# Kernel optimization log

Hardware: AMD Instinct MI355X
Metric: run time of the kernel (lower is better)

Reference implementation:

```python
import jax, jax.numpy as jnp
import numpy as np

NUM_HEADS = 16
ROPE_BASE = 10000.0


def _rope_cos_sin(seq_len, head_dim, dtype):
    inv_freq = 1.0 / (ROPE_BASE ** (jnp.arange(0, head_dim, 2, dtype=jnp.float32) / head_dim))
    freqs = jnp.arange(seq_len, dtype=jnp.float32)[:, None] * inv_freq[None, :]  # [L, hd/2]
    return jnp.cos(freqs).astype(dtype), jnp.sin(freqs).astype(dtype)


def _apply_rope(t, cos, sin):
    # t: [B, H, L, hd]; cos/sin: [L, hd/2] broadcast over B,H
    x1 = t[..., ::2]
    x2 = t[..., 1::2]
    r1 = x1 * cos - x2 * sin
    r2 = x1 * sin + x2 * cos
    return jnp.stack([r1, r2], axis=-1).reshape(t.shape)


def setup_inputs() -> dict:
    key = jax.random.key(0)
    k1, k2, k3 = jax.random.split(key, 3)
    B, L, D = 2, 2048, 1024
    x = jax.random.normal(k1, (B, L, D), dtype=jnp.float32)
    W_qkv = jax.random.normal(k2, (3 * D, D), dtype=jnp.float32) * (D ** -0.5)
    W_out = jax.random.normal(k3, (D, D), dtype=jnp.float32) * (D ** -0.5)
    return {"x": x, "W_qkv": W_qkv, "W_out": W_out}


def reference(x, W_qkv, W_out):
    B, L, D = x.shape
    H = NUM_HEADS
    hd = D // H
    scale = hd ** -0.5

    qkv = x @ W_qkv.T                              # [B, L, 3D]
    qkv = qkv.reshape(B, L, 3, H, hd)
    qkv = jnp.transpose(qkv, (2, 0, 3, 1, 4))      # [3, B, H, L, hd]
    q, k, v = qkv[0], qkv[1], qkv[2]

    cos, sin = _rope_cos_sin(L, hd, x.dtype)
    q = _apply_rope(q, cos, sin)
    k = _apply_rope(k, cos, sin)

    logits = jnp.einsum("bhqd,bhkd->bhqk", q, k) * scale
    attn = jax.nn.softmax(logits, axis=-1)         # dropout p=0.0 -> identity
    out = jnp.einsum("bhqk,bhkd->bhqd", attn, v)   # [B, H, L, hd]
    out = jnp.transpose(out, (0, 2, 1, 3)).reshape(B, L, D)
    return out @ W_out.T
```

## Files before the change

### kernel.cpp

```cpp
#include <hip/hip_runtime.h>
#include <hip/hip_bf16.h>
#include <stdint.h>


typedef __bf16 bf16x8 __attribute__((ext_vector_type(8)));
typedef float f32x4 __attribute__((ext_vector_type(4)));

__device__ __forceinline__ unsigned short f2bf(float f) {
  union { float f; unsigned int u; } v; v.f = f;
  unsigned int r = v.u + 0x7FFFu + ((v.u >> 16) & 1u);
  return (unsigned short)(r >> 16);
}
__device__ __forceinline__ float b2f(unsigned short u) {
  union { unsigned int u; float f; } v; v.u = ((unsigned int)u) << 16;
  return v.f;
}

__device__ __forceinline__ void gl2lds16(const void* gptr, void* lptr) {
  __builtin_amdgcn_global_load_lds(
      (const __attribute__((address_space(1))) unsigned int*)gptr,
      (__attribute__((address_space(3))) unsigned int*)lptr, 16, 0, 0);
}

__global__ void cvt_all(const float4* __restrict__ x,
                        const float4* __restrict__ wq,
                        const float4* __restrict__ wo,
                        ushort4* __restrict__ xb,
                        ushort4* __restrict__ wqb,
                        ushort4* __restrict__ wob) {
  int i = blockIdx.x * 256 + threadIdx.x;
  float4 v; ushort4* dst; int j;
  if (i < 1048576)      { v = x[i];            dst = xb;  j = i; }
  else if (i < 1835008) { v = wq[i - 1048576]; dst = wqb; j = i - 1048576; }
  else                  { v = wo[i - 1835008]; dst = wob; j = i - 1835008; }
  ushort4 o;
  o.x = f2bf(v.x); o.y = f2bf(v.y); o.z = f2bf(v.z); o.w = f2bf(v.w);
  dst[j] = o;
}

template<int OUT_BF16>
__global__ __launch_bounds__(256) void gemm_bt(
    const __hip_bfloat16* __restrict__ A,
    const __hip_bfloat16* __restrict__ B,
    void* __restrict__ C, int M, int N, int K) {
  __shared__ __align__(16) __hip_bfloat16 As[128 * 32];
  __shared__ __align__(16) __hip_bfloat16 Bs[128 * 32];
  const int tid = threadIdx.x;
  const int lane = tid & 63;
  const int wave = tid >> 6;
  const int wm = (wave >> 1) * 64, wn = (wave & 1) * 64;
  const int g = lane >> 4, lr = lane & 15;
  const int m0 = blockIdx.y * 128, n0 = blockIdx.x * 128;
  f32x4 acc[4][4] = {};

  const char* Ag = (const char*)(A + (size_t)m0 * K);
  const char* Bg = (const char*)(B + (size_t)n0 * K);
  const size_t ldb = (size_t)K * 2;

  for (int kt = 0; kt < K; kt += 32) {
    const char* Ak = Ag + (size_t)kt * 2;
    const char* Bk = Bg + (size_t)kt * 2;
#pragma unroll
    for (int j = 0; j < 2; ++j) {
      int c = tid + j * 256;
      int row = c >> 2;
      int colb = (c & 3) * 16;
      gl2lds16(Ak + (size_t)row * ldb + colb, (char*)As + c * 16);
      gl2lds16(Bk + (size_t)row * ldb + colb, (char*)Bs + c * 16);
    }
    asm volatile("s_waitcnt vmcnt(0)" ::: "memory");
    __syncthreads();
    bf16x8 af[4], bfr[4];
#pragma unroll
    for (int i = 0; i < 4; ++i)
      af[i] = *(const bf16x8*)((const char*)As + (size_t)(wm + i * 16 + lr) * 64 + g * 16);
#pragma unroll
    for (int i = 0; i < 4; ++i)
      bfr[i] = *(const bf16x8*)((const char*)Bs + (size_t)(wn + i * 16 + lr) * 64 + g * 16);
#pragma unroll
    for (int i = 0; i < 4; ++i)
#pragma unroll
      for (int j = 0; j < 4; ++j)
        acc[i][j] = __builtin_amdgcn_mfma_f32_16x16x32_bf16(af[i], bfr[j], acc[i][j], 0, 0, 0);
    __syncthreads();
  }

#pragma unroll
  for (int i = 0; i < 4; ++i) {
#pragma unroll
    for (int j = 0; j < 4; ++j) {
      int n = n0 + wn + j * 16 + lr;
#pragma unroll
      for (int r = 0; r < 4; ++r) {
        int m = m0 + wm + i * 16 + g * 4 + r;
        float v = acc[i][j][r];
        if (OUT_BF16) {
          ((unsigned short*)C)[(size_t)m * N + n] = f2bf(v);
        } else {
          ((float*)C)[(size_t)m * N + n] = v;
        }
      }
    }
  }
}

__global__ void rope_scatter(const __hip_bfloat16* __restrict__ qkv,
                             __hip_bfloat16* __restrict__ Qs,
                             __hip_bfloat16* __restrict__ Ks,
                             __hip_bfloat16* __restrict__ Vt) {
  const int t = blockIdx.x * 256 + threadIdx.x;
  const int i = t & 31;
  const int lc = (t >> 5) & 255;
  const int h = (t >> 13) & 15;
  const int b = t >> 17;
  const float inv_freq = powf(10000.0f, -(float)i * (1.0f / 32.0f));
  const float QSCALE = 0.125f * 1.44269504088896f;
  const unsigned short* qk = (const unsigned short*)qkv;
  unsigned short v0[8], v1[8];
#pragma unroll
  for (int j = 0; j < 8; ++j) {
    const int l = lc * 8 + j;
    const size_t row = ((size_t)(b * 2048 + l)) * 3072;
    float s, c;
    sincosf((float)l * inv_freq, &s, &c);
    ushort2 qp = *(const ushort2*)(qk + row + h * 64 + 2 * i);
    ushort2 kp = *(const ushort2*)(qk + row + 1024 + h * 64 + 2 * i);
    ushort2 vp = *(const ushort2*)(qk + row + 2048 + h * 64 + 2 * i);
    float x1 = b2f(qp.x), x2 = b2f(qp.y);
    float y1 = b2f(kp.x), y2 = b2f(kp.y);
    size_t oidx = (((size_t)(b * 16 + h)) * 2048 + l) * 64 + 2 * i;
    ushort2 qo, ko;
    qo.x = f2bf((x1 * c - x2 * s) * QSCALE);
    qo.y = f2bf((x1 * s + x2 * c) * QSCALE);
    ko.x = f2bf(y1 * c - y2 * s);
    ko.y = f2bf(y1 * s + y2 * c);
    *(ushort2*)((unsigned short*)Qs + oidx) = qo;
    *(ushort2*)((unsigned short*)Ks + oidx) = ko;
    v0[j] = vp.x; v1[j] = vp.y;
  }
  const int m = lc & 3;
  const int colA = ((m & 1) << 4) + ((m >> 1) << 2);
  unsigned short* Vtu = (unsigned short*)Vt;
  const size_t vrow0 = (((size_t)(b * 16 + h)) * 64 + 2 * i) * 2048 + (lc >> 2) * 32;
  const size_t vrow1 = vrow0 + 2048;
  *(ushort4*)(Vtu + vrow0 + colA)     = make_ushort4(v0[0], v0[1], v0[2], v0[3]);
  *(ushort4*)(Vtu + vrow0 + colA + 8) = make_ushort4(v0[4], v0[5], v0[6], v0[7]);
  *(ushort4*)(Vtu + vrow1 + colA)     = make_ushort4(v1[0], v1[1], v1[2], v1[3]);
  *(ushort4*)(Vtu + vrow1 + colA + 8) = make_ushort4(v1[4], v1[5], v1[6], v1[7]);
}

__global__ __launch_bounds__(256, 4) void attn_fwd(
    const __hip_bfloat16* __restrict__ Qs,
    const __hip_bfloat16* __restrict__ Ks,
    const __hip_bfloat16* __restrict__ Vt,
    float* __restrict__ Opart,
    float2* __restrict__ Ml) {
  constexpr int L = 2048;
  __shared__ __align__(16) char lds[32768];
  const int tid = threadIdx.x, lane = tid & 63, w = tid >> 6;
  const int g = lane >> 4, lr = lane & 15;
  const int blk = blockIdx.x;
  const int xcd = blk & 7, slot = blk >> 3;
  const int bh = xcd * 4 + (slot >> 5);
  const int rem = slot & 31;
  const int qt = rem >> 1, half = rem & 1;
  const int q0 = qt * 128 + w * 32 + lr;
  const int kt0 = half * 16;

  const __hip_bfloat16* Qr = Qs + ((size_t)bh * L + q0) * 64;
  bf16x8 qf[2][2];
  qf[0][0] = *(const bf16x8*)(Qr + g * 8);
  qf[0][1] = *(const bf16x8*)(Qr + 32 + g * 8);
  qf[1][0] = *(const bf16x8*)(Qr + 16 * 64 + g * 8);
  qf[1][1] = *(const bf16x8*)(Qr + 16 * 64 + 32 + g * 8);

  const int xmask = (lr & 7) << 4;
  const int loff0 = ((g * 16) ^ (xmask & 0x30)) + (xmask & 0x40);
  const int kb0 = lr * 128 + loff0;
  const int kb1 = kb0 ^ 64;

  const int c0 = tid * 16, c1 = c0 + 4096;
  const int os0 = c0 ^ (((c0 >> 7) & 7) << 4);
  const int os1 = c1 ^ (((c1 >> 7) & 7) << 4);
  const char* Kb = (const char*)(Ks + (size_t)bh * L * 64) + (size_t)kt0 * 8192;
  const char* Vb = (const char*)(Vt + (size_t)bh * 64 * L) + kt0 * 128;
  const char* KsrcA = Kb + os0;
  const char* KsrcB = Kb + os1;
  const char* VsrcA = Vb + (size_t)(os0 >> 7) * (L * 2) + (os0 & 127);
  const char* VsrcB = Vb + (size_t)(os1 >> 7) * (L * 2) + (os1 & 127);

  auto stage = [&](int bo) {
    gl2lds16(KsrcA, lds + bo + c0);
    gl2lds16(KsrcB, lds + bo + c1);
    gl2lds16(VsrcA, lds + 16384 + bo + c0);
    gl2lds16(VsrcB, lds + 16384 + bo + c1);
    KsrcA += 8192; KsrcB += 8192; VsrcA += 128; VsrcB += 128;
  };

  f32x4 oacc[2][4] = {};
  float mrun[2] = {-1e30f, -1e30f}, lpart[2] = {0.0f, 0.0f};

  stage(0);

  for (int kt = 0; kt < 16; ++kt) {
    const int bo = (kt & 1) * 8192;
    if (kt + 1 < 16) {
      stage(bo ^ 8192);
      asm volatile("s_waitcnt vmcnt(4)" ::: "memory");
    } else {
      asm volatile("s_waitcnt vmcnt(0)" ::: "memory");
    }
    __builtin_amdgcn_s_barrier();

    const char* Kc = lds + bo;
    const char* Vc = lds + 16384 + bo;

    f32x4 sacc[2][4] = {};
    __builtin_amdgcn_s_setprio(1);
#pragma unroll
    for (int mf = 0; mf < 4; ++mf) {
      bf16x8 a0 = *(const bf16x8*)(Kc + kb0 + mf * 2048);
      bf16x8 a1 = *(const bf16x8*)(Kc + kb1 + mf * 2048);
      sacc[0][mf] = __builtin_amdgcn_mfma_f32_16x16x32_bf16(a0, qf[0][0], sacc[0][mf], 0, 0, 0);
      sacc[0][mf] = __builtin_amdgcn_mfma_f32_16x16x32_bf16(a1, qf[0][1], sacc[0][mf], 0, 0, 0);
      sacc[1][mf] = __builtin_amdgcn_mfma_f32_16x16x32_bf16(a0, qf[1][0], sacc[1][mf], 0, 0, 0);
      sacc[1][mf] = __builtin_amdgcn_mfma_f32_16x16x32_bf16(a1, qf[1][1], sacc[1][mf], 0, 0, 0);
    }
    __builtin_amdgcn_s_setprio(0);

#pragma unroll
    for (int qg = 0; qg < 2; ++qg) {
      float t0 = fmaxf(fmaxf(sacc[qg][0][0], sacc[qg][0][1]), fmaxf(sacc[qg][0][2], sacc[qg][0][3]));
      float t1 = fmaxf(fmaxf(sacc[qg][1][0], sacc[qg][1][1]), fmaxf(sacc[qg][1][2], sacc[qg][1][3]));
      float t2 = fmaxf(fmaxf(sacc[qg][2][0], sacc[qg][2][1]), fmaxf(sacc[qg][2][2], sacc[qg][2][3]));
      float t3 = fmaxf(fmaxf(sacc[qg][3][0], sacc[qg][3][1]), fmaxf(sacc[qg][3][2], sacc[qg][3][3]));
      float tmax = fmaxf(fmaxf(t0, t1), fmaxf(t2, t3));
      tmax = fmaxf(tmax, __shfl_xor(tmax, 16));
      tmax = fmaxf(tmax, __shfl_xor(tmax, 32));
      if (__any(tmax > mrun[qg] + 8.0f)) {
        float mnew = fmaxf(mrun[qg], tmax);
        float al = __builtin_amdgcn_exp2f(mrun[qg] - mnew);
        mrun[qg] = mnew;
        lpart[qg] *= al;
#pragma unroll
        for (int d = 0; d < 4; ++d) oacc[qg][d] = oacc[qg][d] * al;
      }
#pragma unroll
      for (int mf = 0; mf < 4; ++mf) {
        float p0 = __builtin_amdgcn_exp2f(sacc[qg][mf][0] - mrun[qg]);
        float p1 = __builtin_amdgcn_exp2f(sacc[qg][mf][1] - mrun[qg]);
        float p2 = __builtin_amdgcn_exp2f(sacc[qg][mf][2] - mrun[qg]);
        float p3 = __builtin_amdgcn_exp2f(sacc[qg][mf][3] - mrun[qg]);
        lpart[qg] += (p0 + p1) + (p2 + p3);
        sacc[qg][mf][0] = p0; sacc[qg][mf][1] = p1;
        sacc[qg][mf][2] = p2; sacc[qg][mf][3] = p3;
      }
    }

#pragma unroll
    for (int ks = 0; ks < 2; ++ks) {
      bf16x8 pf[2];
#pragma unroll
      for (int qg = 0; qg < 2; ++qg) {
#pragma unroll
        for (int j = 0; j < 4; ++j) {
          pf[qg][j]     = (__bf16)sacc[qg][2 * ks][j];
          pf[qg][4 + j] = (__bf16)sacc[qg][2 * ks + 1][j];
        }
      }
      const int kb = ks ? kb1 : kb0;
      __builtin_amdgcn_s_setprio(1);
#pragma unroll
      for (int df = 0; df < 4; ++df) {
        bf16x8 a = *(const bf16x8*)(Vc + kb + df * 2048);
        oacc[0][df] = __builtin_amdgcn_mfma_f32_16x16x32_bf16(a, pf[0], oacc[0][df], 0, 0, 0);
        oacc[1][df] = __builtin_amdgcn_mfma_f32_16x16x32_bf16(a, pf[1], oacc[1][df], 0, 0, 0);
      }
      __builtin_amdgcn_s_setprio(0);
    }
    asm volatile("s_waitcnt lgkmcnt(0)" ::: "memory");
    __builtin_amdgcn_s_barrier();
  }

#pragma unroll
  for (int qg = 0; qg < 2; ++qg) {
    float lsum = lpart[qg];
    lsum += __shfl_xor(lsum, 16);
    lsum += __shfl_xor(lsum, 32);
    const size_t rowi = ((size_t)bh * L + q0 + qg * 16) * 2 + half;
    float* Od = Opart + rowi * 64;
#pragma unroll
    for (int df = 0; df < 4; ++df)
      *(f32x4*)(Od + df * 16 + g * 4) = oacc[qg][df];
    if (g == 0) {
      float2 ml; ml.x = mrun[qg]; ml.y = lsum;
      Ml[rowi] = ml;
    }
  }
}

__global__ __launch_bounds__(256) void attn_reduce(
    const float* __restrict__ Opart, const float2* __restrict__ Ml,
    unsigned short* __restrict__ Ob) {
  int t = blockIdx.x * 256 + threadIdx.x;
  int d = t & 63;
  int r = t >> 6;
  float2 a = Ml[2 * r], b = Ml[2 * r + 1];
  float m = fmaxf(a.x, b.x);
  float w0 = __builtin_amdgcn_exp2f(a.x - m);
  float w1 = __builtin_amdgcn_exp2f(b.x - m);
  float l = a.y * w0 + b.y * w1;
  float o = Opart[(size_t)(2 * r) * 64 + d] * w0 + Opart[(size_t)(2 * r + 1) * 64 + d] * w1;
  float out = o / l;
  int bh = r >> 11, qq = r & 2047;
  Ob[(((size_t)(bh >> 4) * 2048 + qq)) * 1024 + (bh & 15) * 64 + d] = f2bf(out);
}

extern "C" void kernel_launch(void* const* d_in, const int* in_sizes, int n_in,
                              void* d_out, int out_size, void* d_ws, size_t ws_size,
                              hipStream_t stream) {
  (void)in_sizes; (void)n_in; (void)out_size; (void)ws_size;
  const float* x    = (const float*)d_in[0];
  const float* wqkv = (const float*)d_in[1];
  const float* wout = (const float*)d_in[2];

  char* ws = (char*)d_ws;
  auto* wob   = (__hip_bfloat16*)(ws + ((size_t)0u  << 20));
  auto* Qsb   = (__hip_bfloat16*)(ws + ((size_t)2u  << 20));
  auto* Ob    = (__hip_bfloat16*)(ws + ((size_t)2u  << 20));
  auto* Ksb   = (__hip_bfloat16*)(ws + ((size_t)10u << 20));
  auto* Vtb   = (__hip_bfloat16*)(ws + ((size_t)18u << 20));
  auto* qkvb  = (__hip_bfloat16*)(ws + ((size_t)26u << 20));
  auto* Opart = (float*)         (ws + ((size_t)26u << 20));
  auto* xb    = (__hip_bfloat16*)(ws + ((size_t)50u << 20));
  auto* wqb   = (__hip_bfloat16*)(ws + ((size_t)58u << 20));
  auto* Mlp   = (float2*)        (ws + ((size_t)58u << 20));

  cvt_all<<<8192, 256, 0, stream>>>((const float4*)x, (const float4*)wqkv,
                                    (const float4*)wout,
                                    (ushort4*)xb, (ushort4*)wqb, (ushort4*)wob);
  gemm_bt<1><<<dim3(24, 32), 256, 0, stream>>>(xb, wqb, (void*)qkvb, 4096, 3072, 1024);
  rope_scatter<<<1024, 256, 0, stream>>>(qkvb, Qsb, Ksb, Vtb);
  attn_fwd<<<1024, 256, 0, stream>>>(Qsb, Ksb, Vtb, Opart, Mlp);
  attn_reduce<<<16384, 256, 0, stream>>>(Opart, Mlp, (unsigned short*)Ob);
  gemm_bt<0><<<dim3(8, 32), 256, 0, stream>>>(Ob, wob, d_out, 4096, 1024, 1024);
}
```

Measured before the change: 147.1 us.

## Split-K output projection with atomics and MFMA-based softmax row sums

The output projection GEMM is split into two K halves over a third grid dimension. The halves accumulate into the zeroed fp32 output with atomic adds, which doubles the block count from 256 so more of the device's compute units are busy. In attention, the softmax row-sum is now computed with an extra MFMA against a ones vector instead of per-lane scalar adds and shuffles. The max reduction also skips the cross-lane shuffles unless a rescale is needed. The costs are an added memset, atomic traffic, and bf16-rounded probabilities feeding the denominator.

```diff
diff --git a/kernel.cpp b/kernel.cpp
--- a/kernel.cpp
+++ b/kernel.cpp
@@ -38,11 +38,11 @@
   dst[j] = o;
 }
 
-template<int OUT_BF16>
+template<int OUT_MODE>
 __global__ __launch_bounds__(256) void gemm_bt(
     const __hip_bfloat16* __restrict__ A,
     const __hip_bfloat16* __restrict__ B,
-    void* __restrict__ C, int M, int N, int K) {
+    void* __restrict__ C, int M, int N, int K, int Ksplit) {
   __shared__ __align__(16) __hip_bfloat16 As[128 * 32];
   __shared__ __align__(16) __hip_bfloat16 Bs[128 * 32];
   const int tid = threadIdx.x;
@@ -51,13 +51,14 @@
   const int wm = (wave >> 1) * 64, wn = (wave & 1) * 64;
   const int g = lane >> 4, lr = lane & 15;
   const int m0 = blockIdx.y * 128, n0 = blockIdx.x * 128;
+  const int kbeg = blockIdx.z * Ksplit;
   f32x4 acc[4][4] = {};
 
   const char* Ag = (const char*)(A + (size_t)m0 * K);
   const char* Bg = (const char*)(B + (size_t)n0 * K);
   const size_t ldb = (size_t)K * 2;
 
-  for (int kt = 0; kt < K; kt += 32) {
+  for (int kt = kbeg; kt < kbeg + Ksplit; kt += 32) {
     const char* Ak = Ag + (size_t)kt * 2;
     const char* Bk = Bg + (size_t)kt * 2;
 #pragma unroll
@@ -94,8 +95,10 @@
       for (int r = 0; r < 4; ++r) {
         int m = m0 + wm + i * 16 + g * 4 + r;
         float v = acc[i][j][r];
-        if (OUT_BF16) {
+        if (OUT_MODE == 1) {
           ((unsigned short*)C)[(size_t)m * N + n] = f2bf(v);
+        } else if (OUT_MODE == 2) {
+          unsafeAtomicAdd(&((float*)C)[(size_t)m * N + n], v);
         } else {
           ((float*)C)[(size_t)m * N + n] = v;
         }
@@ -174,6 +177,10 @@
   qf[1][0] = *(const bf16x8*)(Qr + 16 * 64 + g * 8);
   qf[1][1] = *(const bf16x8*)(Qr + 16 * 64 + 32 + g * 8);
 
+  bf16x8 onesf;
+#pragma unroll
+  for (int j = 0; j < 8; ++j) onesf[j] = (__bf16)1.0f;
+
   const int xmask = (lr & 7) << 4;
   const int loff0 = ((g * 16) ^ (xmask & 0x30)) + (xmask & 0x40);
   const int kb0 = lr * 128 + loff0;
@@ -198,7 +205,8 @@
   };
 
   f32x4 oacc[2][4] = {};
-  float mrun[2] = {-1e30f, -1e30f}, lpart[2] = {0.0f, 0.0f};
+  f32x4 lacc[2] = {};
+  float mrun[2] = {-1e30f, -1e30f};
 
   stage(0);
 
@@ -230,30 +238,30 @@
 
 #pragma unroll
     for (int qg = 0; qg < 2; ++qg) {
-      float t0 = fmaxf(fmaxf(sacc[qg][0][0], sacc[qg][0][1]), fmaxf(sacc[qg][0][2], sacc[qg][0][3]));
-      float t1 = fmaxf(fmaxf(sacc[qg][1][0], sacc[qg][1][1]), fmaxf(sacc[qg][1][2], sacc[qg][1][3]));
-      float t2 = fmaxf(fmaxf(sacc[qg][2][0], sacc[qg][2][1]), fmaxf(sacc[qg][2][2], sacc[qg][2][3]));
-      float t3 = fmaxf(fmaxf(sacc[qg][3][0], sacc[qg][3][1]), fmaxf(sacc[qg][3][2], sacc[qg][3][3]));
-      float tmax = fmaxf(fmaxf(t0, t1), fmaxf(t2, t3));
-      tmax = fmaxf(tmax, __shfl_xor(tmax, 16));
-      tmax = fmaxf(tmax, __shfl_xor(tmax, 32));
-      if (__any(tmax > mrun[qg] + 8.0f)) {
+      float a0 = fmaxf(fmaxf(sacc[qg][0][0], sacc[qg][0][1]), sacc[qg][0][2]);
+      float a1 = fmaxf(fmaxf(sacc[qg][0][3], sacc[qg][1][0]), sacc[qg][1][1]);
+      float a2 = fmaxf(fmaxf(sacc[qg][1][2], sacc[qg][1][3]), sacc[qg][2][0]);
+      float a3 = fmaxf(fmaxf(sacc[qg][2][1], sacc[qg][2][2]), sacc[qg][2][3]);
+      float a4 = fmaxf(fmaxf(sacc[qg][3][0], sacc[qg][3][1]), sacc[qg][3][2]);
+      float b0 = fmaxf(fmaxf(a0, a1), a2);
+      float b1 = fmaxf(fmaxf(a3, a4), sacc[qg][3][3]);
+      float lmax = fmaxf(b0, b1);
+      if (__any(lmax > mrun[qg] + 8.0f)) {
+        float tmax = fmaxf(lmax, __shfl_xor(lmax, 16));
+        tmax = fmaxf(tmax, __shfl_xor(tmax, 32));
         float mnew = fmaxf(mrun[qg], tmax);
         float al = __builtin_amdgcn_exp2f(mrun[qg] - mnew);
         mrun[qg] = mnew;
-        lpart[qg] *= al;
+        lacc[qg] *= al;
 #pragma unroll
         for (int d = 0; d < 4; ++d) oacc[qg][d] = oacc[qg][d] * al;
       }
 #pragma unroll
       for (int mf = 0; mf < 4; ++mf) {
-        float p0 = __builtin_amdgcn_exp2f(sacc[qg][mf][0] - mrun[qg]);
-        float p1 = __builtin_amdgcn_exp2f(sacc[qg][mf][1] - mrun[qg]);
-        float p2 = __builtin_amdgcn_exp2f(sacc[qg][mf][2] - mrun[qg]);
-        float p3 = __builtin_amdgcn_exp2f(sacc[qg][mf][3] - mrun[qg]);
-        lpart[qg] += (p0 + p1) + (p2 + p3);
-        sacc[qg][mf][0] = p0; sacc[qg][mf][1] = p1;
-        sacc[qg][mf][2] = p2; sacc[qg][mf][3] = p3;
+        sacc[qg][mf][0] = __builtin_amdgcn_exp2f(sacc[qg][mf][0] - mrun[qg]);
+        sacc[qg][mf][1] = __builtin_amdgcn_exp2f(sacc[qg][mf][1] - mrun[qg]);
+        sacc[qg][mf][2] = __builtin_amdgcn_exp2f(sacc[qg][mf][2] - mrun[qg]);
+        sacc[qg][mf][3] = __builtin_amdgcn_exp2f(sacc[qg][mf][3] - mrun[qg]);
       }
     }
 
@@ -270,6 +278,8 @@
       }
       const int kb = ks ? kb1 : kb0;
       __builtin_amdgcn_s_setprio(1);
+      lacc[0] = __builtin_amdgcn_mfma_f32_16x16x32_bf16(onesf, pf[0], lacc[0], 0, 0, 0);
+      lacc[1] = __builtin_amdgcn_mfma_f32_16x16x32_bf16(onesf, pf[1], lacc[1], 0, 0, 0);
 #pragma unroll
       for (int df = 0; df < 4; ++df) {
         bf16x8 a = *(const bf16x8*)(Vc + kb + df * 2048);
@@ -284,16 +294,13 @@
 
 #pragma unroll
   for (int qg = 0; qg < 2; ++qg) {
-    float lsum = lpart[qg];
-    lsum += __shfl_xor(lsum, 16);
-    lsum += __shfl_xor(lsum, 32);
     const size_t rowi = ((size_t)bh * L + q0 + qg * 16) * 2 + half;
     float* Od = Opart + rowi * 64;
 #pragma unroll
     for (int df = 0; df < 4; ++df)
       *(f32x4*)(Od + df * 16 + g * 4) = oacc[qg][df];
     if (g == 0) {
-      float2 ml; ml.x = mrun[qg]; ml.y = lsum;
+      float2 ml; ml.x = mrun[qg]; ml.y = lacc[qg][0];
       Ml[rowi] = ml;
     }
   }
@@ -319,7 +326,7 @@
 extern "C" void kernel_launch(void* const* d_in, const int* in_sizes, int n_in,
                               void* d_out, int out_size, void* d_ws, size_t ws_size,
                               hipStream_t stream) {
-  (void)in_sizes; (void)n_in; (void)out_size; (void)ws_size;
+  (void)in_sizes; (void)n_in; (void)ws_size;
   const float* x    = (const float*)d_in[0];
   const float* wqkv = (const float*)d_in[1];
   const float* wout = (const float*)d_in[2];
@@ -339,9 +346,12 @@
   cvt_all<<<8192, 256, 0, stream>>>((const float4*)x, (const float4*)wqkv,
                                     (const float4*)wout,
                                     (ushort4*)xb, (ushort4*)wqb, (ushort4*)wob);
-  gemm_bt<1><<<dim3(24, 32), 256, 0, stream>>>(xb, wqb, (void*)qkvb, 4096, 3072, 1024);
+  gemm_bt<1><<<dim3(24, 32, 1), 256, 0, stream>>>(xb, wqb, (void*)qkvb,
+                                                  4096, 3072, 1024, 1024);
   rope_scatter<<<1024, 256, 0, stream>>>(qkvb, Qsb, Ksb, Vtb);
   attn_fwd<<<1024, 256, 0, stream>>>(Qsb, Ksb, Vtb, Opart, Mlp);
   attn_reduce<<<16384, 256, 0, stream>>>(Opart, Mlp, (unsigned short*)Ob);
-  gemm_bt<0><<<dim3(8, 32), 256, 0, stream>>>(Ob, wob, d_out, 4096, 1024, 1024);
-}
+  hipMemsetAsync(d_out, 0, (size_t)out_size * sizeof(float), stream);
+  gemm_bt<2><<<dim3(8, 32, 2), 256, 0, stream>>>(Ob, wob, d_out,
+                                                 4096, 1024, 1024, 512);
+}
```

After: 160.1 us. +8.8%, slower.
